# Kernel optimization log

Measured on AMD Instinct MI355X. Metric: run time of the kernel, lower is better.

## Reference

```python
import jax, jax.numpy as jnp
import numpy as np

N_HEADS = 16


def setup_inputs() -> dict:
    key = jax.random.key(0)
    ks = jax.random.split(key, 10)
    B, M, N, C, D = 2, 2048, 2048, 1024, 1024
    s = 0.02
    return {
        "kv": jax.random.normal(ks[0], (B, M, C), jnp.float32),
        "q": jax.random.normal(ks[1], (B, N, D), jnp.float32),
        "Wk": jax.random.normal(ks[2], (C, D), jnp.float32) * s,
        "bk": jnp.zeros((D,), jnp.float32),
        "Wq": jax.random.normal(ks[3], (D, D), jnp.float32) * s,
        "bq": jnp.zeros((D,), jnp.float32),
        "Wv": jax.random.normal(ks[4], (C, D), jnp.float32) * s,
        "bv": jnp.zeros((D,), jnp.float32),
        "Wp": jax.random.normal(ks[5], (D, D), jnp.float32) * s,
        "bp": jnp.zeros((D,), jnp.float32),
    }


def reference(kv, q, Wk, bk, Wq, bq, Wv, bv, Wp, bp):
    B, M, C = kv.shape
    B2, N, D = q.shape
    H = N_HEADS
    hd = D // H
    # projections (weights stored as [in, out]; torch Linear is x @ W.T + b with W [out,in])
    k = (kv @ Wk + bk).reshape(B, M, H, hd).transpose(0, 2, 1, 3)  # [B,H,M,hd]
    qh = (q @ Wq + bq).reshape(B, N, H, hd).transpose(0, 2, 1, 3)  # [B,H,N,hd]
    v = (kv @ Wv + bv).reshape(B, M, H, hd).transpose(0, 2, 1, 3)  # [B,H,M,hd]
    scale = 1.0 / jnp.sqrt(jnp.asarray(hd, k.dtype))
    att = jnp.einsum("bhnd,bhmd->bhnm", qh, k) * scale
    att = jax.nn.softmax(att, axis=-1)
    y = jnp.einsum("bhnm,bhmd->bhnd", att, v)  # [B,H,N,hd]
    y = y.transpose(0, 2, 1, 3).reshape(B, N, D)
    return y @ Wp + bp
```

## Files before the change

### kernel.cpp

```cpp
#include <hip/hip_runtime.h>

#define DV 1024
#define HD 64

typedef short v4s __attribute__((ext_vector_type(4)));
typedef short v8s __attribute__((ext_vector_type(8)));
typedef float v4f __attribute__((ext_vector_type(4)));

__device__ __forceinline__ short f2bf(float x){
  unsigned u = __float_as_uint(x);
  u += 0x7FFFu + ((u >> 16) & 1u);
  return (short)(u >> 16);
}

__device__ __forceinline__ void async16(const void* g, void* l){
  __builtin_amdgcn_global_load_lds((const __attribute__((address_space(1))) void*)g,
                                   (__attribute__((address_space(3))) void*)l, 16, 0, 0);
}

__device__ __forceinline__ int swz(int lane){
  return (((lane & 7) ^ (lane >> 3)) << 3);
}

__global__ __launch_bounds__(256) void cvt2(const float* __restrict__ xa,
                                            const float* __restrict__ xb,
                                            short* __restrict__ ya,
                                            short* __restrict__ yb, int n){
  const float* x = blockIdx.y ? xb : xa;
  short* y = blockIdx.y ? yb : ya;
  int stride = gridDim.x * 256 * 4;
  for (int i = (blockIdx.x * 256 + threadIdx.x) * 4; i < n; i += stride){
    float4 v = *(const float4*)(x + i);
    v4s s; s.x = f2bf(v.x); s.y = f2bf(v.y); s.z = f2bf(v.z); s.w = f2bf(v.w);
    *(v4s*)(y + i) = s;
  }
}

__global__ __launch_bounds__(256) void tcvt4(
    const float* __restrict__ W0, const float* __restrict__ W1,
    const float* __restrict__ W2, const float* __restrict__ W3,
    short* __restrict__ T0, short* __restrict__ T1,
    short* __restrict__ T2, short* __restrict__ T3){
  const float* W; short* Wt;
  switch (blockIdx.z){
    case 0: W = W0; Wt = T0; break;
    case 1: W = W1; Wt = T1; break;
    case 2: W = W2; Wt = T2; break;
    default: W = W3; Wt = T3; break;
  }
  __shared__ short L[64 * 68];
  const int t = threadIdx.x;
  const int k0 = blockIdx.y * 64, n0 = blockIdx.x * 64;
  const int rr = t >> 4, cc = (t & 15) * 4;
  #pragma unroll
  for (int j = 0; j < 4; j++){
    int r = rr + j * 16;
    float4 v = *(const float4*)(W + (size_t)(k0 + r) * DV + n0 + cc);
    v4s s; s.x = f2bf(v.x); s.y = f2bf(v.y); s.z = f2bf(v.z); s.w = f2bf(v.w);
    *(v4s*)&L[r * 68 + cc] = s;
  }
  __syncthreads();
  #pragma unroll
  for (int j = 0; j < 4; j++){
    int n = rr + j * 16;
    v4s s;
    s.x = L[(cc + 0) * 68 + n];
    s.y = L[(cc + 1) * 68 + n];
    s.z = L[(cc + 2) * 68 + n];
    s.w = L[(cc + 3) * 68 + n];
    *(v4s*)(Wt + (size_t)(n0 + n) * DV + k0 + cc) = s;
  }
}

template<typename OUT_T>
__device__ __forceinline__ void gemm_tile(
    const short* __restrict__ A, const short* __restrict__ Bt,
    const float* __restrict__ bias, OUT_T* __restrict__ C,
    int M, int N, int K, float out_scale, int m0, int n0, bool bias_row)
{
  __shared__ short As[128 * 64];
  __shared__ short Bs[128 * 64];
  const int tid = threadIdx.x;
  const int wave = tid >> 6, lane = tid & 63;
  const int quad = lane >> 4, l15 = lane & 15;
  const int wr = (wave >> 1) * 64, wc = (wave & 1) * 64;
  const int srow = lane >> 3;
  const int sw = swz(lane);
  const v4f vzero = {0.f, 0.f, 0.f, 0.f};

  v4f acc[4][4];
  #pragma unroll
  for (int i = 0; i < 4; i++)
    #pragma unroll
    for (int j = 0; j < 4; j++)
      acc[i][j] = vzero;

  for (int kt = 0; kt < K; kt += 64){
    __syncthreads();
    #pragma unroll
    for (int ii = 0; ii < 4; ii++){
      int i = wave * 4 + ii;
      async16(A  + (size_t)(m0 + i * 8 + srow) * K + kt + sw, &As[i * 512]);
      async16(Bt + (size_t)(n0 + i * 8 + srow) * K + kt + sw, &Bs[i * 512]);
    }
    __syncthreads();
    #pragma unroll
    for (int ks = 0; ks < 2; ks++){
      v8s a[4], b[4];
      #pragma unroll
      for (int mt = 0; mt < 4; mt++)
        a[mt] = *(const v8s*)&As[(wr + mt * 16 + l15) * 64 + (((ks * 4 + quad) ^ (l15 & 7)) << 3)];
      #pragma unroll
      for (int nt = 0; nt < 4; nt++)
        b[nt] = *(const v8s*)&Bs[(wc + nt * 16 + l15) * 64 + (((ks * 4 + quad) ^ (l15 & 7)) << 3)];
      #pragma unroll
      for (int mt = 0; mt < 4; mt++)
        #pragma unroll
        for (int nt = 0; nt < 4; nt++)
          acc[mt][nt] = __builtin_amdgcn_mfma_f32_16x16x32_bf16(a[mt], b[nt], acc[mt][nt], 0, 0, 0);
    }
  }

  #pragma unroll
  for (int mt = 0; mt < 4; mt++){
    #pragma unroll
    for (int nt = 0; nt < 4; nt++){
      int row = m0 + wr + mt * 16 + quad * 4;
      int col = n0 + wc + nt * 16 + l15;
      float bcol = bias_row ? 0.0f : bias[col];
      #pragma unroll
      for (int r = 0; r < 4; r++){
        float bv = bias_row ? bias[row + r] : bcol;
        float v = (acc[mt][nt][r] + bv) * out_scale;
        if (sizeof(OUT_T) == 2)
          ((short*)C)[(size_t)(row + r) * N + col] = f2bf(v);
        else
          ((float*)C)[(size_t)(row + r) * N + col] = v;
      }
    }
  }
}

__global__ __launch_bounds__(256) void proj3(
    const short* __restrict__ qb, const short* __restrict__ kvb,
    const short* __restrict__ Wqt, const short* __restrict__ Wkt,
    const short* __restrict__ Wvt,
    const float* __restrict__ bq, const float* __restrict__ bk,
    const float* __restrict__ bv,
    short* __restrict__ Qp, short* __restrict__ Kp, short* __restrict__ VT,
    float qscale)
{
  int bid = blockIdx.x;
  const short *A, *Bt; const float* bias; short* C;
  int M, N, m0, n0; float scale; bool brow;
  if (bid < 512){
    int z = bid >> 8, l = bid & 255;
    M = 4096; N = 1024; m0 = (l >> 3) * 128; n0 = (l & 7) * 128;
    A = z ? kvb : qb; Bt = z ? Wkt : Wqt; bias = z ? bk : bq;
    C = z ? Kp : Qp; scale = z ? 1.0f : qscale; brow = false;
  } else {
    int l = bid - 512;
    M = 1024; N = 4096; m0 = (l >> 5) * 128; n0 = (l & 31) * 128;
    A = Wvt; Bt = kvb; bias = bv; C = VT; scale = 1.0f; brow = true;
  }
  gemm_tile<short>(A, Bt, bias, C, M, N, 1024, scale, m0, n0, brow);
}

__global__ __launch_bounds__(256) void gemm_f32(
    const short* __restrict__ A, const short* __restrict__ Bt,
    const float* __restrict__ bias, float* __restrict__ C)
{
  gemm_tile<float>(A, Bt, bias, C, 4096, 1024, 1024, 1.0f,
                   blockIdx.y * 128, blockIdx.x * 128, false);
}

__global__ __launch_bounds__(256, 4) void attn(
    const short* __restrict__ Qp, const short* __restrict__ Kp,
    const short* __restrict__ Vt, short* __restrict__ Y)
{
  __shared__ short Qs[64 * 64];
  __shared__ short Ks[64 * 64];
  __shared__ short Vs[64 * 64];
  const int tid = threadIdx.x;
  const int wave = tid >> 6, lane = tid & 63;
  const int quad = lane >> 4, l15 = lane & 15;
  const int n0 = blockIdx.x * 64;
  const int h = blockIdx.y;
  const int b = blockIdx.z;
  const int srow = lane >> 3;
  const int sw = swz(lane);
  const size_t rowbase = (size_t)b * 2048;
  const v4f vzero = {0.f, 0.f, 0.f, 0.f};

  #pragma unroll
  for (int ii = 0; ii < 2; ii++){
    int i = wave * 2 + ii;
    async16(Qp + (rowbase + n0 + i * 8 + srow) * DV + h * HD + sw, &Qs[i * 512]);
  }
  __syncthreads();

  v8s qf[2];
  #pragma unroll
  for (int ks = 0; ks < 2; ks++)
    qf[ks] = *(const v8s*)&Qs[(wave * 16 + l15) * 64 + (((ks * 4 + quad) ^ (l15 & 7)) << 3)];

  v4f o[4];
  #pragma unroll
  for (int dt = 0; dt < 4; dt++) o[dt] = vzero;
  float lsum = 0.0f;

  for (int kt = 0; kt < 32; kt++){
    const int kv0 = kt * 64;
    __syncthreads();
    #pragma unroll
    for (int ii = 0; ii < 2; ii++){
      int i = wave * 2 + ii;
      async16(Kp + (rowbase + kv0 + i * 8 + srow) * DV + h * HD + sw, &Ks[i * 512]);
      async16(Vt + (size_t)(h * HD + i * 8 + srow) * 4096 + rowbase + kv0 + sw, &Vs[i * 512]);
    }
    __syncthreads();

    v4f s[4];
    #pragma unroll
    for (int kvt = 0; kvt < 4; kvt++) s[kvt] = vzero;
    #pragma unroll
    for (int ks = 0; ks < 2; ks++){
      v8s a[4];
      #pragma unroll
      for (int kvt = 0; kvt < 4; kvt++)
        a[kvt] = *(const v8s*)&Ks[(kvt * 16 + l15) * 64 + (((ks * 4 + quad) ^ (l15 & 7)) << 3)];
      #pragma unroll
      for (int kvt = 0; kvt < 4; kvt++)
        s[kvt] = __builtin_amdgcn_mfma_f32_16x16x32_bf16(a[kvt], qf[ks], s[kvt], 0, 0, 0);
    }

    v4s pf[4];
    #pragma unroll
    for (int kvt = 0; kvt < 4; kvt++){
      float p0 = __builtin_amdgcn_exp2f(s[kvt][0]);
      float p1 = __builtin_amdgcn_exp2f(s[kvt][1]);
      float p2 = __builtin_amdgcn_exp2f(s[kvt][2]);
      float p3 = __builtin_amdgcn_exp2f(s[kvt][3]);
      lsum += (p0 + p1) + (p2 + p3);
      v4s pk; pk.x = f2bf(p0); pk.y = f2bf(p1); pk.z = f2bf(p2); pk.w = f2bf(p3);
      pf[kvt] = pk;
    }

    #pragma unroll
    for (int ks = 0; ks < 4; ks++){
      v4s a[4];
      #pragma unroll
      for (int dt = 0; dt < 4; dt++){
        int vc = ks * 16 + quad * 4;
        a[dt] = *(const v4s*)&Vs[(dt * 16 + l15) * 64 + (((vc >> 3) ^ (l15 & 7)) << 3) + (vc & 7)];
      }
      #pragma unroll
      for (int dt = 0; dt < 4; dt++)
        o[dt] = __builtin_amdgcn_mfma_f32_16x16x16bf16_1k(a[dt], pf[ks], o[dt], 0, 0, 0);
    }
  }

  lsum += __shfl_xor(lsum, 16);
  lsum += __shfl_xor(lsum, 32);
  float inv = 1.0f / lsum;
  size_t row = rowbase + n0 + wave * 16 + l15;
  #pragma unroll
  for (int dt = 0; dt < 4; dt++){
    int col = h * HD + dt * 16 + quad * 4;
    unsigned p0 = (unsigned short)f2bf(o[dt][0] * inv) |
                  ((unsigned)(unsigned short)f2bf(o[dt][1] * inv) << 16);
    unsigned p1 = (unsigned short)f2bf(o[dt][2] * inv) |
                  ((unsigned)(unsigned short)f2bf(o[dt][3] * inv) << 16);
    *(unsigned*)(Y + row * DV + col)     = p0;
    *(unsigned*)(Y + row * DV + col + 2) = p1;
  }
}

extern "C" void kernel_launch(void* const* d_in, const int* in_sizes, int n_in,
                              void* d_out, int out_size, void* d_ws, size_t ws_size,
                              hipStream_t stream) {
  const float* kv = (const float*)d_in[0];
  const float* q  = (const float*)d_in[1];
  const float* Wk = (const float*)d_in[2];
  const float* bk = (const float*)d_in[3];
  const float* Wq = (const float*)d_in[4];
  const float* bq = (const float*)d_in[5];
  const float* Wv = (const float*)d_in[6];
  const float* bv = (const float*)d_in[7];
  const float* Wp = (const float*)d_in[8];
  const float* bp = (const float*)d_in[9];

  const size_t E  = 4194304;
  const size_t WE = 1048576;
  short* p   = (short*)d_ws;
  short* kvb = p; p += E;
  short* qb  = p; p += E;
  short* Wkt = p; p += WE;
  short* Wqt = p; p += WE;
  short* Wvt = p; p += WE;
  short* Wpt = p; p += WE;
  short* Kp  = p; p += E;
  short* Qp  = p; p += E;
  short* VT  = p; p += E;
  short* Yb  = p; p += E;

  cvt2<<<dim3(512, 2), 256, 0, stream>>>(kv, q, kvb, qb, (int)E);
  tcvt4<<<dim3(16, 16, 4), 256, 0, stream>>>(Wk, Wq, Wv, Wp, Wkt, Wqt, Wvt, Wpt);

  proj3<<<768, 256, 0, stream>>>(qb, kvb, Wqt, Wkt, Wvt, bq, bk, bv,
                                 Qp, Kp, VT, 0.18033688011f);

  attn<<<dim3(32, 16, 2), 256, 0, stream>>>(Qp, Kp, VT, Yb);

  gemm_f32<<<dim3(8, 32), 256, 0, stream>>>(Yb, Wpt, bp, (float*)d_out);
}
```

Before: 238.7 us.

## Register-prefetch next tiles in GEMM and attention, remap block order

Replaces the synchronous global-to-LDS async loads with a register prefetch: each iteration stores the previously loaded tile into LDS, then issues global loads for the next tile before the MFMA compute, so memory latency overlaps with math. Block index mappings are reordered so consecutive blocks share weight columns (GEMMs) or the same query tile across heads (attention), and launch bounds hint 3 waves per SIMD for the GEMMs. This costs extra VGPRs for the staging registers, which could reduce occupancy.

```diff
diff --git a/kernel.cpp b/kernel.cpp
--- a/kernel.cpp
+++ b/kernel.cpp
@@ -88,6 +88,21 @@
   const int sw = swz(lane);
   const v4f vzero = {0.f, 0.f, 0.f, 0.f};
 
+  const short* pa[4]; const short* pb[4];
+  #pragma unroll
+  for (int ii = 0; ii < 4; ii++){
+    int i = wave * 4 + ii;
+    pa[ii] = A  + (size_t)(m0 + i * 8 + srow) * K + sw;
+    pb[ii] = Bt + (size_t)(n0 + i * 8 + srow) * K + sw;
+  }
+
+  v8s ra[4], rb[4];
+  #pragma unroll
+  for (int ii = 0; ii < 4; ii++){
+    ra[ii] = *(const v8s*)(pa[ii]);
+    rb[ii] = *(const v8s*)(pb[ii]);
+  }
+
   v4f acc[4][4];
   #pragma unroll
   for (int i = 0; i < 4; i++)
@@ -100,10 +115,17 @@
     #pragma unroll
     for (int ii = 0; ii < 4; ii++){
       int i = wave * 4 + ii;
-      async16(A  + (size_t)(m0 + i * 8 + srow) * K + kt + sw, &As[i * 512]);
-      async16(Bt + (size_t)(n0 + i * 8 + srow) * K + kt + sw, &Bs[i * 512]);
+      *(v8s*)&As[i * 512 + lane * 8] = ra[ii];
+      *(v8s*)&Bs[i * 512 + lane * 8] = rb[ii];
     }
     __syncthreads();
+    if (kt + 64 < K){
+      #pragma unroll
+      for (int ii = 0; ii < 4; ii++){
+        ra[ii] = *(const v8s*)(pa[ii] + kt + 64);
+        rb[ii] = *(const v8s*)(pb[ii] + kt + 64);
+      }
+    }
     #pragma unroll
     for (int ks = 0; ks < 2; ks++){
       v8s a[4], b[4];
@@ -141,7 +163,7 @@
   }
 }
 
-__global__ __launch_bounds__(256) void proj3(
+__global__ __launch_bounds__(256, 3) void proj3(
     const short* __restrict__ qb, const short* __restrict__ kvb,
     const short* __restrict__ Wqt, const short* __restrict__ Wkt,
     const short* __restrict__ Wvt,
@@ -155,7 +177,7 @@
   int M, N, m0, n0; float scale; bool brow;
   if (bid < 512){
     int z = bid >> 8, l = bid & 255;
-    M = 4096; N = 1024; m0 = (l >> 3) * 128; n0 = (l & 7) * 128;
+    M = 4096; N = 1024; m0 = (l & 31) * 128; n0 = (l >> 5) * 128;
     A = z ? kvb : qb; Bt = z ? Wkt : Wqt; bias = z ? bk : bq;
     C = z ? Kp : Qp; scale = z ? 1.0f : qscale; brow = false;
   } else {
@@ -166,12 +188,13 @@
   gemm_tile<short>(A, Bt, bias, C, M, N, 1024, scale, m0, n0, brow);
 }
 
-__global__ __launch_bounds__(256) void gemm_f32(
+__global__ __launch_bounds__(256, 3) void gemm_f32(
     const short* __restrict__ A, const short* __restrict__ Bt,
     const float* __restrict__ bias, float* __restrict__ C)
 {
+  int bid = blockIdx.x;
   gemm_tile<float>(A, Bt, bias, C, 4096, 1024, 1024, 1.0f,
-                   blockIdx.y * 128, blockIdx.x * 128, false);
+                   (bid & 31) * 128, (bid >> 5) * 128, false);
 }
 
 __global__ __launch_bounds__(256, 4) void attn(
@@ -184,9 +207,10 @@
   const int tid = threadIdx.x;
   const int wave = tid >> 6, lane = tid & 63;
   const int quad = lane >> 4, l15 = lane & 15;
-  const int n0 = blockIdx.x * 64;
-  const int h = blockIdx.y;
-  const int b = blockIdx.z;
+  const int gid = blockIdx.x;
+  const int qi = gid >> 5, bh = gid & 31;
+  const int h = bh & 15, b = bh >> 4;
+  const int n0 = qi * 64;
   const int srow = lane >> 3;
   const int sw = swz(lane);
   const size_t rowbase = (size_t)b * 2048;
@@ -197,6 +221,18 @@
     int i = wave * 2 + ii;
     async16(Qp + (rowbase + n0 + i * 8 + srow) * DV + h * HD + sw, &Qs[i * 512]);
   }
+
+  const short* pk[2]; const short* pv[2];
+  #pragma unroll
+  for (int ii = 0; ii < 2; ii++){
+    int i = wave * 2 + ii;
+    pk[ii] = Kp + (rowbase + i * 8 + srow) * DV + h * HD + sw;
+    pv[ii] = Vt + (size_t)(h * HD + i * 8 + srow) * 4096 + rowbase + sw;
+  }
+  v8s rk[2], rv[2];
+  #pragma unroll
+  for (int ii = 0; ii < 2; ii++){ rk[ii] = *(const v8s*)(pk[ii]); rv[ii] = *(const v8s*)(pv[ii]); }
+
   __syncthreads();
 
   v8s qf[2];
@@ -210,15 +246,21 @@
   float lsum = 0.0f;
 
   for (int kt = 0; kt < 32; kt++){
-    const int kv0 = kt * 64;
     __syncthreads();
     #pragma unroll
     for (int ii = 0; ii < 2; ii++){
       int i = wave * 2 + ii;
-      async16(Kp + (rowbase + kv0 + i * 8 + srow) * DV + h * HD + sw, &Ks[i * 512]);
-      async16(Vt + (size_t)(h * HD + i * 8 + srow) * 4096 + rowbase + kv0 + sw, &Vs[i * 512]);
+      *(v8s*)&Ks[i * 512 + lane * 8] = rk[ii];
+      *(v8s*)&Vs[i * 512 + lane * 8] = rv[ii];
     }
     __syncthreads();
+    if (kt < 31){
+      #pragma unroll
+      for (int ii = 0; ii < 2; ii++){
+        rk[ii] = *(const v8s*)(pk[ii] + (size_t)(kt + 1) * 64 * DV);
+        rv[ii] = *(const v8s*)(pv[ii] + (kt + 1) * 64);
+      }
+    }
 
     v4f s[4];
     #pragma unroll
@@ -242,8 +284,8 @@
       float p2 = __builtin_amdgcn_exp2f(s[kvt][2]);
       float p3 = __builtin_amdgcn_exp2f(s[kvt][3]);
       lsum += (p0 + p1) + (p2 + p3);
-      v4s pk; pk.x = f2bf(p0); pk.y = f2bf(p1); pk.z = f2bf(p2); pk.w = f2bf(p3);
-      pf[kvt] = pk;
+      v4s pk4; pk4.x = f2bf(p0); pk4.y = f2bf(p1); pk4.z = f2bf(p2); pk4.w = f2bf(p3);
+      pf[kvt] = pk4;
     }
 
     #pragma unroll
@@ -310,7 +352,7 @@
   proj3<<<768, 256, 0, stream>>>(qb, kvb, Wqt, Wkt, Wvt, bq, bk, bv,
                                  Qp, Kp, VT, 0.18033688011f);
 
-  attn<<<dim3(32, 16, 2), 256, 0, stream>>>(Qp, Kp, VT, Yb);
-
-  gemm_f32<<<dim3(8, 32), 256, 0, stream>>>(Yb, Wpt, bp, (float*)d_out);
-}
+  attn<<<1024, 256, 0, stream>>>(Qp, Kp, VT, Yb);
+
+  gemm_f32<<<256, 256, 0, stream>>>(Yb, Wpt, bp, (float*)d_out);
+}
```

New measurement: 216.8 us. 9.2% less time.
